# Kernel optimization log

Measured on AMD Instinct MI355X. Metric: run time of the kernel, lower is better.

Reference implementation:

```python
import jax, jax.numpy as jnp
import numpy as np


def setup_inputs() -> dict:
    key = jax.random.key(0)
    kq, kk = jax.random.split(key)
    B, Q, K, D = 32, 512, 512, 1024
    queries = jax.random.normal(kq, (B, Q, D), dtype=jnp.float32)
    keys = jax.random.normal(kk, (B, K, D), dtype=jnp.float32)
    # ProbabilityConverter learned scalars (is_temperature=True, is_bias=True)
    temperature = jnp.ones((), dtype=jnp.float32)
    bias = jnp.zeros((), dtype=jnp.float32)
    return {"queries": queries, "keys": keys, "temperature": temperature, "bias": bias}


def reference(queries, keys, temperature, bias):
    # Dot scoring: (B, Q, D) x (B, K, D) -> (B, Q, K)
    logits = jnp.einsum("bqd,bkd->bqk", queries, keys)
    # keys.eq(0.0)[:, :, :1].transpose(1, 2): mask positions where first key feature == 0
    key_mask = (keys[:, :, 0] == 0.0)[:, None, :]  # (B, 1, K)
    neg_inf = jnp.array(-jnp.inf, dtype=logits.dtype)
    logits = jnp.where(key_mask, neg_inf, logits)
    # confidence = sigmoid((logsumexp(logits) + bias) * temperature)
    approx_max_logit = jax.nn.logsumexp(logits, axis=-1)  # (B, Q)
    confidence = jax.nn.sigmoid((approx_max_logit + bias) * temperature)
    attn = jax.nn.softmax(logits, axis=-1)  # (B, Q, K)
    return attn, confidence
```

## Files before the change

### kernel.cpp

```cpp
#include <hip/hip_runtime.h>
#include <math.h>
#include <stdint.h>


#define NB 32
#define NQ 512
#define NK 512
#define ND 1024
#define BK 32
#define NT (ND / BK)
#define BM1 64
#define BM3 64
#define TILE_BYTES 65536
#define WS_TILES ((size_t)NB * NT * TILE_BYTES)
#define WS_TOTAL (WS_TILES + (size_t)NB * NK * 4)

typedef __attribute__((ext_vector_type(8))) short short8;
typedef __attribute__((ext_vector_type(4))) float f32x4;

__device__ __forceinline__ void bf_split(float x, unsigned& hbits, float& lo) {
  unsigned u = __float_as_uint(x);
  unsigned r = u + 0x7fffu + ((u >> 16) & 1u);
  hbits = r & 0xffff0000u;
  lo = x - __uint_as_float(hbits);
}
__device__ __forceinline__ unsigned pack_rn(float x0, float x1) {
  unsigned u0 = __float_as_uint(x0), u1 = __float_as_uint(x1);
  unsigned r0 = u0 + 0x7fffu + ((u0 >> 16) & 1u);
  unsigned r1 = u1 + 0x7fffu + ((u1 >> 16) & 1u);
  return (r0 >> 16) | (r1 & 0xffff0000u);
}

__device__ __forceinline__ int lds_off_write(int r, int c4) {
  int slot = ((c4 >> 1) + (r >> 1)) & 3;
  return r * 32 + slot * 8 + (c4 & 1) * 4;
}
__device__ __forceinline__ int lds_off_read(int r, int quad) {
  int slot = (quad + (r >> 1)) & 3;
  return r * 32 + slot * 8;
}

__device__ __forceinline__ void gl2lds16(const void* g, void* l) {
  __builtin_amdgcn_global_load_lds(
      (const __attribute__((address_space(1))) unsigned int*)g,
      (__attribute__((address_space(3))) unsigned int*)l, 16, 0, 0);
}

__global__ __launch_bounds__(256)
void convert_k(const float* __restrict__ Kg, unsigned char* __restrict__ ws) {
  const int bx = blockIdx.x;
  const int batch = bx >> 5, kt = bx & 31;
  const float* src = Kg + (size_t)batch * NK * ND + kt * BK;
  unsigned short* hiB = (unsigned short*)(ws + (size_t)bx * TILE_BYTES);
  unsigned short* loB = hiB + 32768 / 2;
  float* maskB = (float*)(ws + WS_TILES) + batch * NK;

#pragma unroll
  for (int i = 0; i < 16; ++i) {
    int idx = threadIdx.x + 256 * i;
    int r = idx >> 3, c4 = idx & 7;
    float4 v = *(const float4*)(src + (size_t)r * ND + c4 * 4);
    unsigned h0, h1, h2, h3;
    float l0, l1, l2, l3;
    bf_split(v.x, h0, l0); bf_split(v.y, h1, l1);
    bf_split(v.z, h2, l2); bf_split(v.w, h3, l3);
    int off = lds_off_write(r, c4);
    *(uint2*)(&hiB[off]) = make_uint2((h0 >> 16) | h1, (h2 >> 16) | h3);
    *(uint2*)(&loB[off]) = make_uint2(pack_rn(l0, l1), pack_rn(l2, l3));
    if (kt == 0 && c4 == 0) maskB[r] = v.x;
  }
}

__device__ __forceinline__ void stage_a(unsigned short* hiA, unsigned short* loA,
                                        int ar, int ac4, float4 v) {
  unsigned h0, h1, h2, h3;
  float l0, l1, l2, l3;
  bf_split(v.x, h0, l0); bf_split(v.y, h1, l1);
  bf_split(v.z, h2, l2); bf_split(v.w, h3, l3);
  int off = lds_off_write(ar, ac4);
  *(uint2*)(&hiA[off]) = make_uint2((h0 >> 16) | h1, (h2 >> 16) | h3);
  *(uint2*)(&loA[off]) = make_uint2(pack_rn(l0, l1), pack_rn(l2, l3));
}

__device__ __forceinline__ void stage_b(const unsigned char* tb,
                                        unsigned short* hiB, unsigned short* loB,
                                        int w, int ln) {
  int b0 = (w * 64 + ln) * 16;
  int b1 = ((16 + w) * 64 + ln) * 16;
  gl2lds16(tb + b0, ((unsigned char*)hiB) + b0);
  gl2lds16(tb + b1, ((unsigned char*)hiB) + b1);
  gl2lds16(tb + 32768 + b0, ((unsigned char*)loB) + b0);
  gl2lds16(tb + 32768 + b1, ((unsigned char*)loB) + b1);
}

__global__ __launch_bounds__(1024, 4)
void attn_fused_v3(const float* __restrict__ Qg,
                   const unsigned char* __restrict__ ws,
                   const float* __restrict__ Tp, const float* __restrict__ Bp,
                   float* __restrict__ attn, float* __restrict__ conf) {
  __shared__ __align__(16) unsigned short sBhi[2][NK * BK];
  __shared__ __align__(16) unsigned short sBlo[2][NK * BK];
  __shared__ __align__(16) unsigned short sAhi[2][BM3 * BK];
  __shared__ __align__(16) unsigned short sAlo[2][BM3 * BK];
  __shared__ float sRedA[8][BM3];
  __shared__ float sRedB[8][BM3];

  const int tid = threadIdx.x;
  const int g = blockIdx.x;
  const int batch = (g & 7) | (((g >> 3) & 3) << 3);
  const int q0 = (g >> 5) * BM3;
  const int ln = tid & 63, w = tid >> 6;
  const int ln15 = ln & 15, quad = ln >> 4;
  const int wc = w & 7, wr = w >> 3;
  const int row0 = wr * 32, col0 = wc * 64;

  const float* Qp = Qg + ((size_t)batch * NQ + q0) * ND;
  const unsigned char* wsB = ws + (size_t)batch * NT * TILE_BYTES;
  const float* maskB = (const float*)(ws + WS_TILES) + batch * NK;

  f32x4 acc[2][4];
#pragma unroll
  for (int mt = 0; mt < 2; ++mt)
#pragma unroll
    for (int nt = 0; nt < 4; ++nt) acc[mt][nt] = (f32x4){0.f, 0.f, 0.f, 0.f};

  const bool aload = (tid < 512);
  const int ar = tid >> 3, ac4 = tid & 7;

  float4 pa = (float4){0.f, 0.f, 0.f, 0.f};
  if (aload) {
    float4 a0 = *(const float4*)(Qp + (size_t)ar * ND + ac4 * 4);
    stage_a(sAhi[0], sAlo[0], ar, ac4, a0);
    pa = *(const float4*)(Qp + BK + (size_t)ar * ND + ac4 * 4);
  }
  stage_b(wsB, sBhi[0], sBlo[0], w, ln);

  for (int kt = 0; kt < NT; ++kt) {
    const int cur = kt & 1, nxt = cur ^ 1;
    __syncthreads();

    if (kt + 1 < NT) {
      stage_b(wsB + (size_t)(kt + 1) * TILE_BYTES, sBhi[nxt], sBlo[nxt], w, ln);
      if (aload) {
        stage_a(sAhi[nxt], sAlo[nxt], ar, ac4, pa);
        if (kt + 2 < NT)
          pa = *(const float4*)(Qp + (kt + 2) * BK + (size_t)ar * ND + ac4 * 4);
      }
    }

    short8 ahi[2], alo[2];
#pragma unroll
    for (int mt = 0; mt < 2; ++mt) {
      int off = lds_off_read(row0 + mt * 16 + ln15, quad);
      ahi[mt] = *(const short8*)(&sAhi[cur][off]);
      alo[mt] = *(const short8*)(&sAlo[cur][off]);
    }
#pragma unroll
    for (int nt = 0; nt < 4; ++nt) {
      int off = lds_off_read(col0 + nt * 16 + ln15, quad);
      short8 bhi = *(const short8*)(&sBhi[cur][off]);
      short8 blo = *(const short8*)(&sBlo[cur][off]);
#pragma unroll
      for (int mt = 0; mt < 2; ++mt) {
        acc[mt][nt] = __builtin_amdgcn_mfma_f32_16x16x32_bf16(ahi[mt], bhi, acc[mt][nt], 0, 0, 0);
        acc[mt][nt] = __builtin_amdgcn_mfma_f32_16x16x32_bf16(ahi[mt], blo, acc[mt][nt], 0, 0, 0);
        acc[mt][nt] = __builtin_amdgcn_mfma_f32_16x16x32_bf16(alo[mt], bhi, acc[mt][nt], 0, 0, 0);
      }
    }
  }

  const float NEGINF = -__builtin_inff();
  float rm[2][4];
#pragma unroll
  for (int mt = 0; mt < 2; ++mt)
#pragma unroll
    for (int rg = 0; rg < 4; ++rg) rm[mt][rg] = NEGINF;

#pragma unroll
  for (int nt = 0; nt < 4; ++nt) {
    int col = col0 + nt * 16 + ln15;
    bool msk = (maskB[col] == 0.0f);
#pragma unroll
    for (int mt = 0; mt < 2; ++mt)
#pragma unroll
      for (int rg = 0; rg < 4; ++rg) {
        float v = msk ? NEGINF : acc[mt][nt][rg];
        acc[mt][nt][rg] = v;
        rm[mt][rg] = fmaxf(rm[mt][rg], v);
      }
  }
#pragma unroll
  for (int mt = 0; mt < 2; ++mt)
#pragma unroll
    for (int rg = 0; rg < 4; ++rg) {
      float v = rm[mt][rg];
#pragma unroll
      for (int d = 1; d < 16; d <<= 1) v = fmaxf(v, __shfl_xor(v, d, 64));
      rm[mt][rg] = v;
    }
  __syncthreads();
  if (ln15 == 0) {
#pragma unroll
    for (int mt = 0; mt < 2; ++mt)
#pragma unroll
      for (int rg = 0; rg < 4; ++rg)
        sRedA[wc][row0 + mt * 16 + quad * 4 + rg] = rm[mt][rg];
  }
  __syncthreads();

  float gmax[2][4], gsum[2][4];
#pragma unroll
  for (int mt = 0; mt < 2; ++mt)
#pragma unroll
    for (int rg = 0; rg < 4; ++rg) {
      int row = row0 + mt * 16 + quad * 4 + rg;
      float m = sRedA[0][row];
#pragma unroll
      for (int c = 1; c < 8; ++c) m = fmaxf(m, sRedA[c][row]);
      gmax[mt][rg] = m;
      gsum[mt][rg] = 0.f;
    }

#pragma unroll
  for (int nt = 0; nt < 4; ++nt)
#pragma unroll
    for (int mt = 0; mt < 2; ++mt)
#pragma unroll
      for (int rg = 0; rg < 4; ++rg) {
        float e = __expf(acc[mt][nt][rg] - gmax[mt][rg]);
        acc[mt][nt][rg] = e;
        gsum[mt][rg] += e;
      }
#pragma unroll
  for (int mt = 0; mt < 2; ++mt)
#pragma unroll
    for (int rg = 0; rg < 4; ++rg) {
      float v = gsum[mt][rg];
#pragma unroll
      for (int d = 1; d < 16; d <<= 1) v += __shfl_xor(v, d, 64);
      gsum[mt][rg] = v;
    }
  if (ln15 == 0) {
#pragma unroll
    for (int mt = 0; mt < 2; ++mt)
#pragma unroll
      for (int rg = 0; rg < 4; ++rg)
        sRedB[wc][row0 + mt * 16 + quad * 4 + rg] = gsum[mt][rg];
  }
  __syncthreads();
#pragma unroll
  for (int mt = 0; mt < 2; ++mt)
#pragma unroll
    for (int rg = 0; rg < 4; ++rg) {
      int row = row0 + mt * 16 + quad * 4 + rg;
      float s = sRedB[0][row];
#pragma unroll
      for (int c = 1; c < 8; ++c) s += sRedB[c][row];
      gsum[mt][rg] = s;
    }

  float* outBase = attn + ((size_t)batch * NQ + q0) * NK;
#pragma unroll
  for (int mt = 0; mt < 2; ++mt)
#pragma unroll
    for (int rg = 0; rg < 4; ++rg) {
      int row = row0 + mt * 16 + quad * 4 + rg;
      float inv = 1.0f / gsum[mt][rg];
#pragma unroll
      for (int nt = 0; nt < 4; ++nt)
        outBase[(size_t)row * NK + col0 + nt * 16 + ln15] = acc[mt][nt][rg] * inv;
    }

  if (wc == 0 && ln15 == 0) {
    float tv = Tp[0], bv = Bp[0];
#pragma unroll
    for (int mt = 0; mt < 2; ++mt)
#pragma unroll
      for (int rg = 0; rg < 4; ++rg) {
        int row = row0 + mt * 16 + quad * 4 + rg;
        float lse = gmax[mt][rg] + __logf(gsum[mt][rg]);
        float t = (lse + bv) * tv;
        conf[(size_t)batch * NQ + q0 + row] = 1.0f / (1.0f + __expf(-t));
      }
  }
}

__global__ __launch_bounds__(256, 1)
void attn_fused_v1(const float* __restrict__ Qg, const float* __restrict__ Kg,
                   const float* __restrict__ Tp, const float* __restrict__ Bp,
                   float* __restrict__ attn, float* __restrict__ conf) {
  __shared__ __align__(16) unsigned short sAhi[BM1 * BK];
  __shared__ __align__(16) unsigned short sAlo[BM1 * BK];
  __shared__ __align__(16) unsigned short sBhi[NK * BK];
  __shared__ __align__(16) unsigned short sBlo[NK * BK];
  __shared__ float sRedA[4][BM1];
  __shared__ float sRedB[4][BM1];

  const int tid = threadIdx.x;
  const int g = blockIdx.x;
  const int batch = (g & 7) | (((g >> 3) & 3) << 3);
  const int q0 = (g >> 5) * BM1;
  const int ln = tid & 63, w = tid >> 6;
  const int ln15 = ln & 15, quad = ln >> 4;
  const int wn0 = w * 128;

  const float* Qp = Qg + ((size_t)batch * NQ + q0) * ND;
  const float* Kp = Kg + (size_t)batch * NK * ND;

  f32x4 acc[4][8];
#pragma unroll
  for (int mt = 0; mt < 4; ++mt)
#pragma unroll
    for (int nt = 0; nt < 8; ++nt) acc[mt][nt] = (f32x4){0.f, 0.f, 0.f, 0.f};

  float4 pb[16], pa[2];
#pragma unroll
  for (int i = 0; i < 16; ++i) {
    int idx = tid + 256 * i, r = idx >> 3, c4 = idx & 7;
    pb[i] = *(const float4*)(Kp + (size_t)r * ND + c4 * 4);
  }
#pragma unroll
  for (int i = 0; i < 2; ++i) {
    int idx = tid + 256 * i, r = idx >> 3, c4 = idx & 7;
    pa[i] = *(const float4*)(Qp + (size_t)r * ND + c4 * 4);
  }

  for (int kt = 0; kt < NT; ++kt) {
    if (kt) __syncthreads();
#pragma unroll
    for (int i = 0; i < 2; ++i) {
      int idx = tid + 256 * i, r = idx >> 3, c4 = idx & 7;
      int off = lds_off_write(r, c4);
      unsigned h0, h1, h2, h3; float l0, l1, l2, l3;
      bf_split(pa[i].x, h0, l0); bf_split(pa[i].y, h1, l1);
      bf_split(pa[i].z, h2, l2); bf_split(pa[i].w, h3, l3);
      *(uint2*)(&sAhi[off]) = make_uint2((h0 >> 16) | h1, (h2 >> 16) | h3);
      *(uint2*)(&sAlo[off]) = make_uint2(pack_rn(l0, l1), pack_rn(l2, l3));
    }
#pragma unroll
    for (int i = 0; i < 16; ++i) {
      int idx = tid + 256 * i, r = idx >> 3, c4 = idx & 7;
      int off = lds_off_write(r, c4);
      unsigned h0, h1, h2, h3; float l0, l1, l2, l3;
      bf_split(pb[i].x, h0, l0); bf_split(pb[i].y, h1, l1);
      bf_split(pb[i].z, h2, l2); bf_split(pb[i].w, h3, l3);
      *(uint2*)(&sBhi[off]) = make_uint2((h0 >> 16) | h1, (h2 >> 16) | h3);
      *(uint2*)(&sBlo[off]) = make_uint2(pack_rn(l0, l1), pack_rn(l2, l3));
    }
    __syncthreads();

    if (kt < NT - 1) {
      const float* Kq = Kp + (kt + 1) * BK;
      const float* Qq = Qp + (kt + 1) * BK;
#pragma unroll
      for (int i = 0; i < 16; ++i) {
        int idx = tid + 256 * i, r = idx >> 3, c4 = idx & 7;
        pb[i] = *(const float4*)(Kq + (size_t)r * ND + c4 * 4);
      }
#pragma unroll
      for (int i = 0; i < 2; ++i) {
        int idx = tid + 256 * i, r = idx >> 3, c4 = idx & 7;
        pa[i] = *(const float4*)(Qq + (size_t)r * ND + c4 * 4);
      }
    }

    short8 ahi[4], alo[4];
#pragma unroll
    for (int mt = 0; mt < 4; ++mt) {
      int off = lds_off_read(mt * 16 + ln15, quad);
      ahi[mt] = *(const short8*)(&sAhi[off]);
      alo[mt] = *(const short8*)(&sAlo[off]);
    }
#pragma unroll
    for (int nt = 0; nt < 8; ++nt) {
      int off = lds_off_read(wn0 + nt * 16 + ln15, quad);
      short8 bhi = *(const short8*)(&sBhi[off]);
      short8 blo = *(const short8*)(&sBlo[off]);
#pragma unroll
      for (int mt = 0; mt < 4; ++mt) {
        acc[mt][nt] = __builtin_amdgcn_mfma_f32_16x16x32_bf16(ahi[mt], bhi, acc[mt][nt], 0, 0, 0);
        acc[mt][nt] = __builtin_amdgcn_mfma_f32_16x16x32_bf16(ahi[mt], blo, acc[mt][nt], 0, 0, 0);
        acc[mt][nt] = __builtin_amdgcn_mfma_f32_16x16x32_bf16(alo[mt], bhi, acc[mt][nt], 0, 0, 0);
      }
    }
  }

  const float NEGINF = -__builtin_inff();
  float rm[4][4];
#pragma unroll
  for (int mt = 0; mt < 4; ++mt)
#pragma unroll
    for (int rg = 0; rg < 4; ++rg) rm[mt][rg] = NEGINF;
#pragma unroll
  for (int nt = 0; nt < 8; ++nt) {
    int col = wn0 + nt * 16 + ln15;
    bool msk = (Kp[(size_t)col * ND] == 0.0f);
#pragma unroll
    for (int mt = 0; mt < 4; ++mt)
#pragma unroll
      for (int rg = 0; rg < 4; ++rg) {
        float v = msk ? NEGINF : acc[mt][nt][rg];
        acc[mt][nt][rg] = v;
        rm[mt][rg] = fmaxf(rm[mt][rg], v);
      }
  }
#pragma unroll
  for (int mt = 0; mt < 4; ++mt)
#pragma unroll
    for (int rg = 0; rg < 4; ++rg) {
      float v = rm[mt][rg];
#pragma unroll
      for (int d = 1; d < 16; d <<= 1) v = fmaxf(v, __shfl_xor(v, d, 64));
      rm[mt][rg] = v;
    }
  if (ln15 == 0)
#pragma unroll
    for (int mt = 0; mt < 4; ++mt)
#pragma unroll
      for (int rg = 0; rg < 4; ++rg)
        sRedA[w][mt * 16 + quad * 4 + rg] = rm[mt][rg];
  __syncthreads();

  float gmax[4][4], gsum[4][4];
#pragma unroll
  for (int mt = 0; mt < 4; ++mt)
#pragma unroll
    for (int rg = 0; rg < 4; ++rg) {
      int row = mt * 16 + quad * 4 + rg;
      gmax[mt][rg] = fmaxf(fmaxf(sRedA[0][row], sRedA[1][row]),
                           fmaxf(sRedA[2][row], sRedA[3][row]));
      gsum[mt][rg] = 0.f;
    }
#pragma unroll
  for (int nt = 0; nt < 8; ++nt)
#pragma unroll
    for (int mt = 0; mt < 4; ++mt)
#pragma unroll
      for (int rg = 0; rg < 4; ++rg) {
        float e = __expf(acc[mt][nt][rg] - gmax[mt][rg]);
        acc[mt][nt][rg] = e;
        gsum[mt][rg] += e;
      }
#pragma unroll
  for (int mt = 0; mt < 4; ++mt)
#pragma unroll
    for (int rg = 0; rg < 4; ++rg) {
      float v = gsum[mt][rg];
#pragma unroll
      for (int d = 1; d < 16; d <<= 1) v += __shfl_xor(v, d, 64);
      gsum[mt][rg] = v;
    }
  if (ln15 == 0)
#pragma unroll
    for (int mt = 0; mt < 4; ++mt)
#pragma unroll
      for (int rg = 0; rg < 4; ++rg)
        sRedB[w][mt * 16 + quad * 4 + rg] = gsum[mt][rg];
  __syncthreads();
#pragma unroll
  for (int mt = 0; mt < 4; ++mt)
#pragma unroll
    for (int rg = 0; rg < 4; ++rg) {
      int row = mt * 16 + quad * 4 + rg;
      gsum[mt][rg] = sRedB[0][row] + sRedB[1][row] + sRedB[2][row] + sRedB[3][row];
    }

  float* outBase = attn + ((size_t)batch * NQ + q0) * NK;
#pragma unroll
  for (int mt = 0; mt < 4; ++mt)
#pragma unroll
    for (int rg = 0; rg < 4; ++rg) {
      int row = mt * 16 + quad * 4 + rg;
      float inv = 1.0f / gsum[mt][rg];
#pragma unroll
      for (int nt = 0; nt < 8; ++nt)
        outBase[(size_t)row * NK + wn0 + nt * 16 + ln15] = acc[mt][nt][rg] * inv;
    }
  if (w == 0 && ln15 == 0) {
    float tv = Tp[0], bv = Bp[0];
#pragma unroll
    for (int mt = 0; mt < 4; ++mt)
#pragma unroll
      for (int rg = 0; rg < 4; ++rg) {
        int row = mt * 16 + quad * 4 + rg;
        float lse = gmax[mt][rg] + __logf(gsum[mt][rg]);
        float t = (lse + bv) * tv;
        conf[(size_t)batch * NQ + q0 + row] = 1.0f / (1.0f + __expf(-t));
      }
  }
}

extern "C" void kernel_launch(void* const* d_in, const int* in_sizes, int n_in,
                              void* d_out, int out_size, void* d_ws, size_t ws_size,
                              hipStream_t stream) {
  const float* q = (const float*)d_in[0];
  const float* k = (const float*)d_in[1];
  const float* temp = (const float*)d_in[2];
  const float* bias = (const float*)d_in[3];
  float* attn = (float*)d_out;
  float* conf = attn + (size_t)NB * NQ * NK;

  if (ws_size >= WS_TOTAL) {
    hipLaunchKernelGGL(convert_k, dim3(NB * NT), dim3(256), 0, stream,
                       k, (unsigned char*)d_ws);
    hipLaunchKernelGGL(attn_fused_v3, dim3(NB * (NQ / BM3)), dim3(1024), 0, stream,
                       q, (const unsigned char*)d_ws, temp, bias, attn, conf);
  } else {
    hipLaunchKernelGGL(attn_fused_v1, dim3(NB * (NQ / BM1)), dim3(256), 0, stream,
                       q, k, temp, bias, attn, conf);
  }
}
```

Before: 220.1 us.

## Load pre-split K tiles straight into registers, drop LDS staging for B

The fused kernel now uses 512 threads (8 waves, each owning 64 key columns and all 64 query rows), with launch bounds of 2 blocks per CU. Each wave loads its B hi/lo fragments directly from the precomputed workspace into registers, double-buffered across an unrolled pair of iterations, instead of staging them through LDS with global_load_lds. This removes the large B LDS buffers and their LDS reads, and raises per-wave MFMA reuse from 2x4 to 4x4 tiles. The costs are higher register pressure and every wave re-reading its B slice from global/L2, while the convert kernel now writes tiles without swizzling.

```diff
diff --git a/kernel.cpp b/kernel.cpp
--- a/kernel.cpp
+++ b/kernel.cpp
@@ -10,7 +10,7 @@
 #define BK 32
 #define NT (ND / BK)
 #define BM1 64
-#define BM3 64
+#define BM4 64
 #define TILE_BYTES 65536
 #define WS_TILES ((size_t)NB * NT * TILE_BYTES)
 #define WS_TOTAL (WS_TILES + (size_t)NB * NK * 4)
@@ -38,12 +38,6 @@
 __device__ __forceinline__ int lds_off_read(int r, int quad) {
   int slot = (quad + (r >> 1)) & 3;
   return r * 32 + slot * 8;
-}
-
-__device__ __forceinline__ void gl2lds16(const void* g, void* l) {
-  __builtin_amdgcn_global_load_lds(
-      (const __attribute__((address_space(1))) unsigned int*)g,
-      (__attribute__((address_space(3))) unsigned int*)l, 16, 0, 0);
 }
 
 __global__ __launch_bounds__(256)
@@ -58,16 +52,16 @@
 #pragma unroll
   for (int i = 0; i < 16; ++i) {
     int idx = threadIdx.x + 256 * i;
-    int r = idx >> 3, c4 = idx & 7;
-    float4 v = *(const float4*)(src + (size_t)r * ND + c4 * 4);
+    int c = idx >> 3, c4 = idx & 7;
+    float4 v = *(const float4*)(src + (size_t)c * ND + c4 * 4);
     unsigned h0, h1, h2, h3;
     float l0, l1, l2, l3;
     bf_split(v.x, h0, l0); bf_split(v.y, h1, l1);
     bf_split(v.z, h2, l2); bf_split(v.w, h3, l3);
-    int off = lds_off_write(r, c4);
+    int off = c * 32 + c4 * 4;
     *(uint2*)(&hiB[off]) = make_uint2((h0 >> 16) | h1, (h2 >> 16) | h3);
     *(uint2*)(&loB[off]) = make_uint2(pack_rn(l0, l1), pack_rn(l2, l3));
-    if (kt == 0 && c4 == 0) maskB[r] = v.x;
+    if (kt == 0 && c4 == 0) maskB[c] = v.x;
   }
 }
 
@@ -82,97 +76,91 @@
   *(uint2*)(&loA[off]) = make_uint2(pack_rn(l0, l1), pack_rn(l2, l3));
 }
 
-__device__ __forceinline__ void stage_b(const unsigned char* tb,
-                                        unsigned short* hiB, unsigned short* loB,
-                                        int w, int ln) {
-  int b0 = (w * 64 + ln) * 16;
-  int b1 = ((16 + w) * 64 + ln) * 16;
-  gl2lds16(tb + b0, ((unsigned char*)hiB) + b0);
-  gl2lds16(tb + b1, ((unsigned char*)hiB) + b1);
-  gl2lds16(tb + 32768 + b0, ((unsigned char*)loB) + b0);
-  gl2lds16(tb + 32768 + b1, ((unsigned char*)loB) + b1);
-}
-
-__global__ __launch_bounds__(1024, 4)
-void attn_fused_v3(const float* __restrict__ Qg,
+#define MFMA_BF16 __builtin_amdgcn_mfma_f32_16x16x32_bf16
+
+#define BODY(KT, CURB, NXTB, CUR, NXT)                                         \
+  do {                                                                         \
+    short8 ahi[4], alo[4];                                                     \
+    _Pragma("unroll") for (int mt = 0; mt < 4; ++mt) {                         \
+      int off = lds_off_read(mt * 16 + ln15, quad);                            \
+      ahi[mt] = *(const short8*)(&sAhi[CUR][off]);                             \
+      alo[mt] = *(const short8*)(&sAlo[CUR][off]);                             \
+    }                                                                          \
+    if ((KT) + 1 < NT) {                                                       \
+      const unsigned char* tb = wsB + (size_t)((KT) + 1) * TILE_BYTES;         \
+      _Pragma("unroll") for (int nt = 0; nt < 4; ++nt) {                       \
+        NXTB[2 * nt]     = *(const float4*)(tb + nt * 1024 + boff);            \
+        NXTB[2 * nt + 1] = *(const float4*)(tb + 32768 + nt * 1024 + boff);    \
+      }                                                                        \
+      stage_a(sAhi[NXT], sAlo[NXT], ar, ac4, pa);                              \
+      if ((KT) + 2 < NT)                                                       \
+        pa = *(const float4*)(Qp + ((KT) + 2) * BK + (size_t)ar * ND + ac4 * 4);\
+    }                                                                          \
+    _Pragma("unroll") for (int nt = 0; nt < 4; ++nt) {                         \
+      short8 bhi = *(const short8*)(&CURB[2 * nt]);                            \
+      short8 blo = *(const short8*)(&CURB[2 * nt + 1]);                        \
+      _Pragma("unroll") for (int mt = 0; mt < 4; ++mt) {                       \
+        acc[mt][nt] = MFMA_BF16(ahi[mt], bhi, acc[mt][nt], 0, 0, 0);           \
+        acc[mt][nt] = MFMA_BF16(ahi[mt], blo, acc[mt][nt], 0, 0, 0);           \
+        acc[mt][nt] = MFMA_BF16(alo[mt], bhi, acc[mt][nt], 0, 0, 0);           \
+      }                                                                        \
+    }                                                                          \
+    asm volatile("s_waitcnt lgkmcnt(0)" ::: "memory");                         \
+    __builtin_amdgcn_s_barrier();                                              \
+  } while (0)
+
+__global__ __launch_bounds__(512, 2)
+void attn_fused_v4(const float* __restrict__ Qg,
                    const unsigned char* __restrict__ ws,
                    const float* __restrict__ Tp, const float* __restrict__ Bp,
                    float* __restrict__ attn, float* __restrict__ conf) {
-  __shared__ __align__(16) unsigned short sBhi[2][NK * BK];
-  __shared__ __align__(16) unsigned short sBlo[2][NK * BK];
-  __shared__ __align__(16) unsigned short sAhi[2][BM3 * BK];
-  __shared__ __align__(16) unsigned short sAlo[2][BM3 * BK];
-  __shared__ float sRedA[8][BM3];
-  __shared__ float sRedB[8][BM3];
+  __shared__ __align__(16) unsigned short sAhi[2][BM4 * BK];
+  __shared__ __align__(16) unsigned short sAlo[2][BM4 * BK];
+  __shared__ __align__(16) float sRedA[BM4][8];
+  __shared__ __align__(16) float sRedB[BM4][8];
 
   const int tid = threadIdx.x;
   const int g = blockIdx.x;
   const int batch = (g & 7) | (((g >> 3) & 3) << 3);
-  const int q0 = (g >> 5) * BM3;
+  const int q0 = (g >> 5) * BM4;
   const int ln = tid & 63, w = tid >> 6;
   const int ln15 = ln & 15, quad = ln >> 4;
-  const int wc = w & 7, wr = w >> 3;
-  const int row0 = wr * 32, col0 = wc * 64;
+  const int col0 = w * 64;
 
   const float* Qp = Qg + ((size_t)batch * NQ + q0) * ND;
   const unsigned char* wsB = ws + (size_t)batch * NT * TILE_BYTES;
   const float* maskB = (const float*)(ws + WS_TILES) + batch * NK;
 
-  f32x4 acc[2][4];
-#pragma unroll
-  for (int mt = 0; mt < 2; ++mt)
+  const int boff = (col0 << 6) + (ln15 << 6) + (quad << 4);
+  const int ar = tid >> 3, ac4 = tid & 7;
+
+  f32x4 acc[4][4];
+#pragma unroll
+  for (int mt = 0; mt < 4; ++mt)
 #pragma unroll
     for (int nt = 0; nt < 4; ++nt) acc[mt][nt] = (f32x4){0.f, 0.f, 0.f, 0.f};
 
-  const bool aload = (tid < 512);
-  const int ar = tid >> 3, ac4 = tid & 7;
-
-  float4 pa = (float4){0.f, 0.f, 0.f, 0.f};
-  if (aload) {
-    float4 a0 = *(const float4*)(Qp + (size_t)ar * ND + ac4 * 4);
-    stage_a(sAhi[0], sAlo[0], ar, ac4, a0);
-    pa = *(const float4*)(Qp + BK + (size_t)ar * ND + ac4 * 4);
-  }
-  stage_b(wsB, sBhi[0], sBlo[0], w, ln);
-
-  for (int kt = 0; kt < NT; ++kt) {
-    const int cur = kt & 1, nxt = cur ^ 1;
-    __syncthreads();
-
-    if (kt + 1 < NT) {
-      stage_b(wsB + (size_t)(kt + 1) * TILE_BYTES, sBhi[nxt], sBlo[nxt], w, ln);
-      if (aload) {
-        stage_a(sAhi[nxt], sAlo[nxt], ar, ac4, pa);
-        if (kt + 2 < NT)
-          pa = *(const float4*)(Qp + (kt + 2) * BK + (size_t)ar * ND + ac4 * 4);
-      }
-    }
-
-    short8 ahi[2], alo[2];
-#pragma unroll
-    for (int mt = 0; mt < 2; ++mt) {
-      int off = lds_off_read(row0 + mt * 16 + ln15, quad);
-      ahi[mt] = *(const short8*)(&sAhi[cur][off]);
-      alo[mt] = *(const short8*)(&sAlo[cur][off]);
-    }
-#pragma unroll
-    for (int nt = 0; nt < 4; ++nt) {
-      int off = lds_off_read(col0 + nt * 16 + ln15, quad);
-      short8 bhi = *(const short8*)(&sBhi[cur][off]);
-      short8 blo = *(const short8*)(&sBlo[cur][off]);
-#pragma unroll
-      for (int mt = 0; mt < 2; ++mt) {
-        acc[mt][nt] = __builtin_amdgcn_mfma_f32_16x16x32_bf16(ahi[mt], bhi, acc[mt][nt], 0, 0, 0);
-        acc[mt][nt] = __builtin_amdgcn_mfma_f32_16x16x32_bf16(ahi[mt], blo, acc[mt][nt], 0, 0, 0);
-        acc[mt][nt] = __builtin_amdgcn_mfma_f32_16x16x32_bf16(alo[mt], bhi, acc[mt][nt], 0, 0, 0);
-      }
-    }
+  float4 a0 = *(const float4*)(Qp + (size_t)ar * ND + ac4 * 4);
+  stage_a(sAhi[0], sAlo[0], ar, ac4, a0);
+  float4 pa = *(const float4*)(Qp + BK + (size_t)ar * ND + ac4 * 4);
+  float4 pbA[8], pbB[8];
+#pragma unroll
+  for (int nt = 0; nt < 4; ++nt) {
+    pbA[2 * nt]     = *(const float4*)(wsB + nt * 1024 + boff);
+    pbA[2 * nt + 1] = *(const float4*)(wsB + 32768 + nt * 1024 + boff);
+  }
+  asm volatile("s_waitcnt lgkmcnt(0)" ::: "memory");
+  __builtin_amdgcn_s_barrier();
+
+  for (int kt = 0; kt < NT; kt += 2) {
+    BODY(kt, pbA, pbB, 0, 1);
+    BODY(kt + 1, pbB, pbA, 1, 0);
   }
 
   const float NEGINF = -__builtin_inff();
-  float rm[2][4];
-#pragma unroll
-  for (int mt = 0; mt < 2; ++mt)
+  float rm[4][4];
+#pragma unroll
+  for (int mt = 0; mt < 4; ++mt)
 #pragma unroll
     for (int rg = 0; rg < 4; ++rg) rm[mt][rg] = NEGINF;
 
@@ -181,7 +169,7 @@
     int col = col0 + nt * 16 + ln15;
     bool msk = (maskB[col] == 0.0f);
 #pragma unroll
-    for (int mt = 0; mt < 2; ++mt)
+    for (int mt = 0; mt < 4; ++mt)
 #pragma unroll
       for (int rg = 0; rg < 4; ++rg) {
         float v = msk ? NEGINF : acc[mt][nt][rg];
@@ -190,7 +178,7 @@
       }
   }
 #pragma unroll
-  for (int mt = 0; mt < 2; ++mt)
+  for (int mt = 0; mt < 4; ++mt)
 #pragma unroll
     for (int rg = 0; rg < 4; ++rg) {
       float v = rm[mt][rg];
@@ -198,33 +186,32 @@
       for (int d = 1; d < 16; d <<= 1) v = fmaxf(v, __shfl_xor(v, d, 64));
       rm[mt][rg] = v;
     }
+  if (ln15 == 0) {
+#pragma unroll
+    for (int mt = 0; mt < 4; ++mt)
+#pragma unroll
+      for (int rg = 0; rg < 4; ++rg)
+        sRedA[mt * 16 + quad * 4 + rg][w] = rm[mt][rg];
+  }
   __syncthreads();
-  if (ln15 == 0) {
-#pragma unroll
-    for (int mt = 0; mt < 2; ++mt)
-#pragma unroll
-      for (int rg = 0; rg < 4; ++rg)
-        sRedA[wc][row0 + mt * 16 + quad * 4 + rg] = rm[mt][rg];
-  }
-  __syncthreads();
-
-  float gmax[2][4], gsum[2][4];
-#pragma unroll
-  for (int mt = 0; mt < 2; ++mt)
-#pragma unroll
-    for (int rg = 0; rg < 4; ++rg) {
-      int row = row0 + mt * 16 + quad * 4 + rg;
-      float m = sRedA[0][row];
-#pragma unroll
-      for (int c = 1; c < 8; ++c) m = fmaxf(m, sRedA[c][row]);
-      gmax[mt][rg] = m;
+
+  float gmax[4][4], gsum[4][4];
+#pragma unroll
+  for (int mt = 0; mt < 4; ++mt)
+#pragma unroll
+    for (int rg = 0; rg < 4; ++rg) {
+      int row = mt * 16 + quad * 4 + rg;
+      f32x4 p0 = *(const f32x4*)(&sRedA[row][0]);
+      f32x4 p1 = *(const f32x4*)(&sRedA[row][4]);
+      gmax[mt][rg] = fmaxf(fmaxf(fmaxf(p0[0], p0[1]), fmaxf(p0[2], p0[3])),
+                           fmaxf(fmaxf(p1[0], p1[1]), fmaxf(p1[2], p1[3])));
       gsum[mt][rg] = 0.f;
     }
 
 #pragma unroll
   for (int nt = 0; nt < 4; ++nt)
 #pragma unroll
-    for (int mt = 0; mt < 2; ++mt)
+    for (int mt = 0; mt < 4; ++mt)
 #pragma unroll
       for (int rg = 0; rg < 4; ++rg) {
         float e = __expf(acc[mt][nt][rg] - gmax[mt][rg]);
@@ -232,7 +219,7 @@
         gsum[mt][rg] += e;
       }
 #pragma unroll
-  for (int mt = 0; mt < 2; ++mt)
+  for (int mt = 0; mt < 4; ++mt)
 #pragma unroll
     for (int rg = 0; rg < 4; ++rg) {
       float v = gsum[mt][rg];
@@ -242,42 +229,42 @@
     }
   if (ln15 == 0) {
 #pragma unroll
-    for (int mt = 0; mt < 2; ++mt)
+    for (int mt = 0; mt < 4; ++mt)
 #pragma unroll
       for (int rg = 0; rg < 4; ++rg)
-        sRedB[wc][row0 + mt * 16 + quad * 4 + rg] = gsum[mt][rg];
+        sRedB[mt * 16 + quad * 4 + rg][w] = gsum[mt][rg];
   }
   __syncthreads();
 #pragma unroll
-  for (int mt = 0; mt < 2; ++mt)
-#pragma unroll
-    for (int rg = 0; rg < 4; ++rg) {
-      int row = row0 + mt * 16 + quad * 4 + rg;
-      float s = sRedB[0][row];
-#pragma unroll
-      for (int c = 1; c < 8; ++c) s += sRedB[c][row];
-      gsum[mt][rg] = s;
+  for (int mt = 0; mt < 4; ++mt)
+#pragma unroll
+    for (int rg = 0; rg < 4; ++rg) {
+      int row = mt * 16 + quad * 4 + rg;
+      f32x4 p0 = *(const f32x4*)(&sRedB[row][0]);
+      f32x4 p1 = *(const f32x4*)(&sRedB[row][4]);
+      gsum[mt][rg] = (p0[0] + p0[1]) + (p0[2] + p0[3]) +
+                     ((p1[0] + p1[1]) + (p1[2] + p1[3]));
     }
 
   float* outBase = attn + ((size_t)batch * NQ + q0) * NK;
 #pragma unroll
-  for (int mt = 0; mt < 2; ++mt)
-#pragma unroll
-    for (int rg = 0; rg < 4; ++rg) {
-      int row = row0 + mt * 16 + quad * 4 + rg;
+  for (int mt = 0; mt < 4; ++mt)
+#pragma unroll
+    for (int rg = 0; rg < 4; ++rg) {
+      int row = mt * 16 + quad * 4 + rg;
       float inv = 1.0f / gsum[mt][rg];
 #pragma unroll
       for (int nt = 0; nt < 4; ++nt)
         outBase[(size_t)row * NK + col0 + nt * 16 + ln15] = acc[mt][nt][rg] * inv;
     }
 
-  if (wc == 0 && ln15 == 0) {
+  if (w == 0 && ln15 == 0) {
     float tv = Tp[0], bv = Bp[0];
 #pragma unroll
-    for (int mt = 0; mt < 2; ++mt)
-#pragma unroll
-      for (int rg = 0; rg < 4; ++rg) {
-        int row = row0 + mt * 16 + quad * 4 + rg;
+    for (int mt = 0; mt < 4; ++mt)
+#pragma unroll
+      for (int rg = 0; rg < 4; ++rg) {
+        int row = mt * 16 + quad * 4 + rg;
         float lse = gmax[mt][rg] + __logf(gsum[mt][rg]);
         float t = (lse + bv) * tv;
         conf[(size_t)batch * NQ + q0 + row] = 1.0f / (1.0f + __expf(-t));
@@ -378,9 +365,9 @@
       short8 blo = *(const short8*)(&sBlo[off]);
 #pragma unroll
       for (int mt = 0; mt < 4; ++mt) {
-        acc[mt][nt] = __builtin_amdgcn_mfma_f32_16x16x32_bf16(ahi[mt], bhi, acc[mt][nt], 0, 0, 0);
-        acc[mt][nt] = __builtin_amdgcn_mfma_f32_16x16x32_bf16(ahi[mt], blo, acc[mt][nt], 0, 0, 0);
-        acc[mt][nt] = __builtin_amdgcn_mfma_f32_16x16x32_bf16(alo[mt], bhi, acc[mt][nt], 0, 0, 0);
+        acc[mt][nt] = MFMA_BF16(ahi[mt], bhi, acc[mt][nt], 0, 0, 0);
+        acc[mt][nt] = MFMA_BF16(ahi[mt], blo, acc[mt][nt], 0, 0, 0);
+        acc[mt][nt] = MFMA_BF16(alo[mt], bhi, acc[mt][nt], 0, 0, 0);
       }
     }
   }
@@ -503,7 +490,7 @@
   if (ws_size >= WS_TOTAL) {
     hipLaunchKernelGGL(convert_k, dim3(NB * NT), dim3(256), 0, stream,
                        k, (unsigned char*)d_ws);
-    hipLaunchKernelGGL(attn_fused_v3, dim3(NB * (NQ / BM3)), dim3(1024), 0, stream,
+    hipLaunchKernelGGL(attn_fused_v4, dim3(NB * (NQ / BM4)), dim3(512), 0, stream,
                        q, (const unsigned char*)d_ws, temp, bias, attn, conf);
   } else {
     hipLaunchKernelGGL(attn_fused_v1, dim3(NB * (NQ / BM1)), dim3(256), 0, stream,
```

Result: faster. 212.5 us (-3.5%).
